# Optimization experiments

Hardware: AMD Instinct MI355X
Metric: run time of the kernel (lower is better)

The kernel has to match this reference:

```python
import jax, jax.numpy as jnp
import numpy as np

NEG_INF = -1e30

def dwconv1(x, dw, db, pw, pb):
    # DWConv with kernel_size=1: depthwise = per-channel scale+bias, pointwise = dense linear.
    # x: [B, L, H]
    return (x * dw + db) @ pw.T + pb

def masked_softmax(logits, maskf, axis):
    # masked_softmax as in SQuAD repos: mask*logits + (1-mask)*(-1e30), then softmax over axis
    m = maskf * logits + (1.0 - maskf) * NEG_INF
    return jax.nn.softmax(m, axis=axis)

def setup_inputs() -> dict:
    key = jax.random.key(0)
    ks = jax.random.split(key, 20)
    B, L, H = 4, 4096, 1024
    s = 1.0 / np.sqrt(H)
    inp = {
        "x": jax.random.normal(ks[0], (B, L, H), dtype=jnp.float32),
        "mask": jax.random.randint(ks[1], (B, L), 0, 2, dtype=jnp.int32),
    }
    names = ["k", "q", "v", "r"]
    for i, n in enumerate(names):
        inp[n + "_dw"] = jax.random.normal(ks[2 + 4 * i], (H,), dtype=jnp.float32) * 0.1 + 1.0
        inp[n + "_db"] = jnp.zeros((H,), dtype=jnp.float32)
        inp[n + "_pw"] = jax.random.normal(ks[3 + 4 * i], (H, H), dtype=jnp.float32) * s
        inp[n + "_pb"] = jnp.zeros((H,), dtype=jnp.float32)
    return inp

def reference(x, mask, k_dw, k_db, k_pw, k_pb, q_dw, q_db, q_pw, q_pb,
              v_dw, v_db, v_pw, v_pb, r_dw, r_db, r_pw, r_pb):
    B, L, H = x.shape
    n_head = 16
    hc = H // n_head
    maskf = mask.astype(x.dtype)[:, None, None, :]  # [B,1,1,L]

    def heads(t):  # [B,L,H] -> [B,nh,hc,L]
        return t.reshape(B, L, n_head, hc).transpose(0, 2, 3, 1)

    keys = heads(dwconv1(x, k_dw, k_db, k_pw, k_pb))
    queries = heads(dwconv1(x, q_dw, q_db, q_pw, q_pb))
    values = heads(dwconv1(x, v_dw, v_db, v_pw, v_pb))

    key_sm = masked_softmax(keys, maskf, axis=3)      # softmax over L
    query_sm = masked_softmax(queries, maskf, axis=2)  # softmax over head channels

    # context = key @ value^T : [B,nh,hc,hc]
    context = jnp.einsum("bhcl,bhdl->bhcd", key_sm, values)
    # attended = context^T @ query : [B,nh,hc(value),L]
    attended = jnp.einsum("bhcd,bhcl->bhdl", context, query_sm)

    agg = attended.transpose(0, 3, 1, 2).reshape(B, L, H)  # concat heads, [B,L,H]
    # dropout is identity in eval mode
    return dwconv1(agg, r_dw, r_db, r_pw, r_pb)
```

## Files before the change

### kernel.cpp

```cpp
#include <hip/hip_runtime.h>
#include <stdint.h>

#define H 1024
#define LSEQ 4096
#define NBATCH 4
#define MT (NBATCH*LSEQ)

typedef __attribute__((ext_vector_type(8))) short bf16x8;
typedef __attribute__((ext_vector_type(4))) short s16x4;
typedef __attribute__((ext_vector_type(4))) float f32x4;

static __device__ __forceinline__ unsigned short f2bf(float f){
  union { float f; unsigned u; } v; v.f = f;
  unsigned u = v.u;
  return (unsigned short)((u + 0x7FFFu + ((u >> 16) & 1u)) >> 16);
}
static __device__ __forceinline__ float bf2f(unsigned short h){
  union { unsigned u; float f; } v; v.u = ((unsigned)h) << 16;
  return v.f;
}
static __device__ __forceinline__ void g2l16(const void* g, void* l){
  __builtin_amdgcn_global_load_lds((const __attribute__((address_space(1))) void*)g,
                                   (__attribute__((address_space(3))) void*)l, 16, 0, 0);
}
static __device__ __forceinline__ f32x4 mfma16(bf16x8 a, bf16x8 b, f32x4 c){
  return __builtin_amdgcn_mfma_f32_16x16x32_bf16(a, b, c, 0, 0, 0);
}

struct P4 { const float* pw[4]; const float* dw[4]; const float* db[4]; const float* pb[4]; };

__global__ __launch_bounds__(256) void prepcvt(P4 a, const float* __restrict__ x,
    short* __restrict__ wb, float* __restrict__ bo, short* __restrict__ xb){
  const int bid = blockIdx.x, t = threadIdx.x;
  if (bid < 4096){
    __shared__ float red[256];
    const int p = bid >> 10, j = bid & 1023;
    const float* row = a.pw[p] + (size_t)j * H;
    const float* dwp = a.dw[p];
    const float* dbp = a.db[p];
    float acc = 0.f;
    #pragma unroll
    for (int k = 0; k < 4; ++k){
      int i = k*256 + t;
      float pv = row[i];
      wb[((size_t)p*H + j)*H + i] = (short)f2bf(pv * dwp[i]);
      acc += dbp[i] * pv;
    }
    red[t] = acc; __syncthreads();
    for (int s = 128; s > 0; s >>= 1){
      if (t < s) red[t] += red[t+s];
      __syncthreads();
    }
    if (t == 0) bo[p*H + j] = a.pb[p][j] + red[0];
  } else {
    const size_t base = ((size_t)(bid - 4096) * 4096) + (size_t)t * 16;
    #pragma unroll
    for (int h2 = 0; h2 < 2; ++h2){
      const float4* p = (const float4*)(x + base + h2*8);
      float4 u = p[0], v = p[1];
      bf16x8 o;
      o[0]=(short)f2bf(u.x); o[1]=(short)f2bf(u.y); o[2]=(short)f2bf(u.z); o[3]=(short)f2bf(u.w);
      o[4]=(short)f2bf(v.x); o[5]=(short)f2bf(v.y); o[6]=(short)f2bf(v.z); o[7]=(short)f2bf(v.w);
      *(bf16x8*)(xb + base + h2*8) = o;
    }
  }
}

template<int MODE, int NBLK>
__global__ __launch_bounds__(512, 2) void gemm8(const short* __restrict__ A,
    const short* __restrict__ WBp, const float* __restrict__ bia,
    short* __restrict__ oq, short* __restrict__ okT, short* __restrict__ ovT,
    float* __restrict__ ofin){
  __shared__ __align__(16) short lsm[2][2][256*64];

  const int nwg = NBLK * 64;
  const int cpx = nwg >> 3;
  const int bid = blockIdx.x;
  const int swz = (bid & 7) * cpx + (bid >> 3);
  const int mb = swz / NBLK, nb = swz % NBLK;
  const int m0 = mb * 256, n0 = nb * 256;

  const int tid  = threadIdx.x;
  const int lane = tid & 63;
  const int w    = tid >> 6;
  const int wm   = w >> 2, wn = w & 3;
  const int q4 = lane >> 4, r16 = lane & 15;
  const int rl = lane >> 3, sl = lane & 7;
  const int srcsw = ((sl ^ rl) << 3);

#define STAGE_A(BUF_, Q_, KB_) \
  g2l16(A + (size_t)(m0 + (Q_)*64 + w*8 + rl)*H + (KB_) + srcsw, \
        &lsm[0][BUF_][((Q_)*64 + w*8)*64])
#define STAGE_B(BUF_, Q_, KB_) \
  g2l16(WBp + (size_t)(n0 + (Q_)*64 + w*8 + rl)*H + (KB_) + srcsw, \
        &lsm[1][BUF_][((Q_)*64 + w*8)*64])
#define RD_A(dst, BUF_, MI8, KK) { const int row_ = wm*128 + (MI8)*16 + r16; \
  dst = *(const bf16x8*)&lsm[0][BUF_][row_*64 + ((((KK)*4+q4) ^ (row_&7))<<3)]; }
#define RD_B(dst, BUF_, NI4, KK) { const int row_ = wn*64 + (NI4)*16 + r16; \
  dst = *(const bf16x8*)&lsm[1][BUF_][row_*64 + ((((KK)*4+q4) ^ (row_&7))<<3)]; }

  f32x4 acc[8][4] = {};
  bf16x8 aF[4][2], bFa[2][2], bFb[2][2];

  STAGE_B(0,0,0); STAGE_B(0,1,0); STAGE_B(0,2,0); STAGE_B(0,3,0);
  STAGE_A(0,0,0); STAGE_A(0,2,0); STAGE_A(0,1,0); STAGE_A(0,3,0);
  asm volatile("s_waitcnt vmcnt(2)" ::: "memory");
  __builtin_amdgcn_s_barrier();

  #pragma unroll 2
  for (int t = 0; t < 16; ++t){
    const int buf = t & 1, sbuf = buf ^ 1;
    const int skb = ((t < 15) ? (t + 1) : 15) << 6;

    #pragma unroll
    for (int mi = 0; mi < 4; ++mi){ RD_A(aF[mi][0], buf, mi, 0); RD_A(aF[mi][1], buf, mi, 1); }
    #pragma unroll
    for (int ni = 0; ni < 2; ++ni){ RD_B(bFa[ni][0], buf, ni, 0); RD_B(bFa[ni][1], buf, ni, 1); }
    #pragma unroll
    for (int ni = 0; ni < 2; ++ni){ RD_B(bFb[ni][0], buf, 2+ni, 0); RD_B(bFb[ni][1], buf, 2+ni, 1); }
    STAGE_B(sbuf, 0, skb); STAGE_B(sbuf, 1, skb);
    STAGE_B(sbuf, 2, skb); STAGE_B(sbuf, 3, skb);
    __builtin_amdgcn_s_setprio(1);
    #pragma unroll
    for (int kk = 0; kk < 2; ++kk)
      #pragma unroll
      for (int mi = 0; mi < 4; ++mi){
        #pragma unroll
        for (int ni = 0; ni < 2; ++ni)
          acc[mi][ni] = mfma16(aF[mi][kk], bFa[ni][kk], acc[mi][ni]);
        #pragma unroll
        for (int ni = 0; ni < 2; ++ni)
          acc[mi][2+ni] = mfma16(aF[mi][kk], bFb[ni][kk], acc[mi][2+ni]);
      }
    __builtin_amdgcn_s_setprio(0);
    asm volatile("s_waitcnt vmcnt(4)" ::: "memory");
    __builtin_amdgcn_s_barrier();

    #pragma unroll
    for (int mi = 0; mi < 4; ++mi){ RD_A(aF[mi][0], buf, 4+mi, 0); RD_A(aF[mi][1], buf, 4+mi, 1); }
    STAGE_A(sbuf, 0, skb); STAGE_A(sbuf, 2, skb);
    STAGE_A(sbuf, 1, skb); STAGE_A(sbuf, 3, skb);
    __builtin_amdgcn_s_setprio(1);
    #pragma unroll
    for (int kk = 0; kk < 2; ++kk)
      #pragma unroll
      for (int mi = 0; mi < 4; ++mi){
        #pragma unroll
        for (int ni = 0; ni < 2; ++ni)
          acc[4+mi][ni] = mfma16(aF[mi][kk], bFa[ni][kk], acc[4+mi][ni]);
        #pragma unroll
        for (int ni = 0; ni < 2; ++ni)
          acc[4+mi][2+ni] = mfma16(aF[mi][kk], bFb[ni][kk], acc[4+mi][2+ni]);
      }
    __builtin_amdgcn_s_setprio(0);
    asm volatile("s_waitcnt vmcnt(2)" ::: "memory");
    __builtin_amdgcn_s_barrier();
  }
#undef STAGE_A
#undef STAGE_B
#undef RD_A
#undef RD_B

  if (MODE == 1){
    #pragma unroll
    for (int ni4 = 0; ni4 < 4; ++ni4){
      const int n = n0 + wn*64 + ni4*16 + r16;
      const float bv = bia[n];
      #pragma unroll
      for (int mi8 = 0; mi8 < 8; ++mi8){
        const int mbse = m0 + wm*128 + mi8*16 + q4*4;
        #pragma unroll
        for (int j = 0; j < 4; ++j)
          ofin[(size_t)(mbse+j)*H + n] = acc[mi8][ni4][j] + bv;
      }
    }
  } else {
    const int p = n0 >> 10;
    if (p == 1){
      #pragma unroll
      for (int ni4 = 0; ni4 < 4; ++ni4){
        const int n = n0 + wn*64 + ni4*16 + r16;
        const float bv = bia[n];
        const int ch = n & 1023;
        #pragma unroll
        for (int mi8 = 0; mi8 < 8; ++mi8){
          const int mbse = m0 + wm*128 + mi8*16 + q4*4;
          #pragma unroll
          for (int j = 0; j < 4; ++j)
            oq[(size_t)(mbse+j)*H + ch] = (short)f2bf(acc[mi8][ni4][j] + bv);
        }
      }
    } else {
      asm volatile("s_waitcnt vmcnt(0)" ::: "memory");
      __syncthreads();
      char* sC = (char*)&lsm[0][0][0];
      #pragma unroll
      for (int ni4 = 0; ni4 < 4; ++ni4){
        const int cr = wn*64 + ni4*16 + r16;
        const float bv = bia[n0 + cr];
        #pragma unroll
        for (int mi8 = 0; mi8 < 8; ++mi8){
          const int s8 = wm*32 + mi8*4 + q4;
          s16x4 v;
          #pragma unroll
          for (int j = 0; j < 4; ++j) v[j] = (short)f2bf(acc[mi8][ni4][j] + bv);
          *(s16x4*)(sC + cr*512 + ((s8 ^ ((cr & 7) << 1)) << 3)) = v;
        }
      }
      __syncthreads();
      short* ot = (p == 0) ? okT : ovT;
      const int ch0 = n0 & 1023, bb = m0 >> 12, lp0 = m0 & 4095;
      const int c = lane & 31;
      #pragma unroll
      for (int it = 0; it < 16; ++it){
        const int cr = it*16 + w*2 + (lane >> 5);
        bf16x8 vv = *(bf16x8*)(sC + cr*512 + ((c ^ (cr & 7)) << 4));
        *(bf16x8*)&ot[((size_t)bb*H + ch0 + cr)*LSEQ + lp0 + c*8] = vv;
      }
    }
  }
}

__global__ __launch_bounds__(512) void ctx_k(const short* __restrict__ kT,
    const short* __restrict__ vT, const int* __restrict__ mask,
    float* __restrict__ ctxP, float* __restrict__ dloc){
  const int lc = blockIdx.x, h = blockIdx.y, b = blockIdx.z;
  __shared__ __align__(16) short lK[2][64*64];
  __shared__ __align__(16) short lV[2][64*64];
  __shared__ float sDenP[8][64];
  __shared__ int sMkG[2][64];
  __shared__ float sAcc[64][65];
  const int tid = threadIdx.x, lane = tid & 63, w = tid >> 6;
  const int grp = w >> 2, wg = w & 3, tig = tid & 255;
  const short* kb = kT + (size_t)(b*16 + h)*64*LSEQ;
  const short* vb = vT + (size_t)(b*16 + h)*64*LSEQ;
  const int l0 = lc*512;

  f32x4 acc[4] = {};
  float dsum = 0.f;
  const int sl = lane & 7, rl = lane >> 3;
  const int lsw = ((sl ^ rl) << 3);
  for (int kc2 = 0; kc2 < 4; ++kc2){
    const int kc = kc2*2 + grp;
    __syncthreads();
    const int lb = l0 + kc*64;
    #pragma unroll
    for (int c = 0; c < 2; ++c){
      const int r = (wg*2+c)*8 + rl;
      g2l16(kb + (size_t)r*LSEQ + lb + lsw, &lK[grp][(wg*2+c)*512]);
      g2l16(vb + (size_t)r*LSEQ + lb + lsw, &lV[grp][(wg*2+c)*512]);
    }
    if (tig < 64) sMkG[grp][tig] = mask[(size_t)b*LSEQ + lb + tig];
    __syncthreads();
    {
      const int row = lane;
      #pragma unroll
      for (int k2 = 0; k2 < 2; ++k2){
        const int slog = wg*2 + k2;
        const int sp = slog ^ (row & 7);
        bf16x8 v = *(bf16x8*)&lK[grp][row*64 + (sp<<3)];
        bf16x8 o;
        #pragma unroll
        for (int e=0;e<8;++e){
          const float f = bf2f((unsigned short)v[e]);
          const float we = sMkG[grp][slog*8+e] ? __expf(f - 8.0f) : 0.0f;
          dsum += we;
          o[e] = (short)f2bf(we);
        }
        *(bf16x8*)&lK[grp][row*64 + (sp<<3)] = o;
      }
    }
    __syncthreads();
    const int q4 = lane >> 4, r16 = lane & 15;
    #pragma unroll
    for (int kk = 0; kk < 2; ++kk){
      const int slog = kk*4 + q4;
      const int rowA = wg*16 + r16;
      bf16x8 a = *(bf16x8*)&lK[grp][rowA*64 + ((slog ^ (rowA & 7))<<3)];
      #pragma unroll
      for (int ni = 0; ni < 4; ++ni){
        const int rowB = ni*16 + r16;
        bf16x8 bv = *(bf16x8*)&lV[grp][rowB*64 + ((slog ^ (rowB & 7))<<3)];
        acc[ni] = mfma16(a, bv, acc[ni]);
      }
    }
  }
  const int q4 = lane >> 4, r16 = lane & 15;
  sDenP[w][lane] = dsum;
  if (grp == 0){
    #pragma unroll
    for (int ni=0;ni<4;++ni){
      const int d = ni*16 + r16;
      #pragma unroll
      for (int j=0;j<4;++j)
        sAcc[wg*16 + q4*4 + j][d] = acc[ni][j];
    }
  }
  __syncthreads();
  if (grp == 1){
    float* op = ctxP + (((size_t)(b*16 + h)*8 + lc) << 12);
    #pragma unroll
    for (int ni=0;ni<4;++ni){
      const int d = ni*16 + r16;
      #pragma unroll
      for (int j=0;j<4;++j){
        const int c = wg*16 + q4*4 + j;
        op[c*64 + d] = acc[ni][j] + sAcc[c][d];
      }
    }
  }
  if (tid < 64){
    const int idx = (((b*16 + h)*8 + lc) << 6) + tid;
    float dv = 0.f;
    #pragma unroll
    for (int ww = 0; ww < 8; ++ww) dv += sDenP[ww][tid];
    dloc[idx] = dv;
  }
}

__global__ __launch_bounds__(512) void attd_k(const short* __restrict__ qb,
    const float* __restrict__ ctxP, const float* __restrict__ dloc,
    const int* __restrict__ mask, short* __restrict__ agg){
  const int lcb = blockIdx.x, h = blockIdx.y, b = blockIdx.z;
  __shared__ __align__(16) short lQ[2][64*64];
  __shared__ __align__(16) short lCt[64*64];
  __shared__ float sInv[64];
  const int tid = threadIdx.x, lane = tid & 63, w = tid >> 6;
  const int grp = w >> 2, wg = w & 3;
  if (tid < 64){
    const int base = ((b*16 + h) << 9) + tid;
    float den = 0.f;
    #pragma unroll
    for (int i = 0; i < 8; ++i) den += dloc[base + i*64];
    sInv[tid] = 1.0f / fmaxf(den, 1e-30f);
  }
  __syncthreads();
  {
    const int d = lane;
    const float* base = ctxP + ((size_t)(b*16 + h)*8 << 12);
    #pragma unroll
    for (int i=0;i<8;++i){
      const int c = w*8 + i;
      float s = 0.f;
      #pragma unroll
      for (int ch = 0; ch < 8; ++ch)
        s += base[ch*4096 + c*64 + d];
      s *= sInv[c];
      lCt[d*64 + ((((c>>3) ^ (d&7))<<3) | (c&7))] = (short)f2bf(s);
    }
  }
  const int l0g = b*LSEQ + lcb*1024 + grp*512;
  const int sl = lane & 7, rl = lane >> 3;
  const int lsw = ((sl ^ rl) << 3);
  for (int sc = 0; sc < 8; ++sc){
    __syncthreads();
    #pragma unroll
    for (int c = 0; c < 2; ++c){
      const int r = (wg*2+c)*8 + rl;
      g2l16(qb + (size_t)(l0g + sc*64 + r)*H + h*64 + lsw, &lQ[grp][(wg*2+c)*512]);
    }
    __syncthreads();
    {
      const int row = wg*16 + (lane & 15);
      const int q4 = lane >> 4;
      const int mk = mask[(size_t)l0g + sc*64 + row];
      float vals[16];
      float mxv = -3e38f;
      #pragma unroll
      for (int k2=0;k2<2;++k2){
        const int slog = q4*2 + k2;
        const int sp = slog ^ (row & 7);
        bf16x8 v = *(bf16x8*)&lQ[grp][row*64 + (sp<<3)];
        #pragma unroll
        for (int e=0;e<8;++e){
          const float f = bf2f((unsigned short)v[e]);
          vals[k2*8+e] = f;
          mxv = fmaxf(mxv, f);
        }
      }
      mxv = fmaxf(mxv, __shfl_xor(mxv, 16));
      mxv = fmaxf(mxv, __shfl_xor(mxv, 32));
      float s = 0.f;
      #pragma unroll
      for (int e=0;e<16;++e){ vals[e] = __expf(vals[e]-mxv); s += vals[e]; }
      s += __shfl_xor(s, 16);
      s += __shfl_xor(s, 32);
      const float inv = 1.0f / s;
      #pragma unroll
      for (int k2=0;k2<2;++k2){
        const int slog = q4*2 + k2;
        const int sp = slog ^ (row & 7);
        bf16x8 o;
        #pragma unroll
        for (int e=0;e<8;++e)
          o[e] = (short)f2bf(mk ? vals[k2*8+e]*inv : 0.015625f);
        *(bf16x8*)&lQ[grp][row*64 + (sp<<3)] = o;
      }
    }
    __syncthreads();
    f32x4 acc[4] = {};
    const int q4 = lane >> 4, r16 = lane & 15;
    #pragma unroll
    for (int kk=0;kk<2;++kk){
      const int slog = kk*4 + q4;
      const int rowA = wg*16 + r16;
      bf16x8 a = *(bf16x8*)&lQ[grp][rowA*64 + ((slog ^ (rowA&7))<<3)];
      #pragma unroll
      for (int ni=0;ni<4;++ni){
        const int rowB = ni*16 + r16;
        bf16x8 bv = *(bf16x8*)&lCt[rowB*64 + ((slog ^ (rowB&7))<<3)];
        acc[ni] = mfma16(a, bv, acc[ni]);
      }
    }
    #pragma unroll
    for (int ni=0;ni<4;++ni){
      const int d = ni*16 + r16;
      #pragma unroll
      for (int j=0;j<4;++j){
        const int lrow = wg*16 + q4*4 + j;
        agg[(size_t)(l0g + sc*64 + lrow)*H + h*64 + d] = (short)f2bf(acc[ni][j]);
      }
    }
  }
}

extern "C" void kernel_launch(void* const* d_in, const int* in_sizes, int n_in,
                              void* d_out, int out_size, void* d_ws, size_t ws_size,
                              hipStream_t stream){
  (void)in_sizes; (void)n_in; (void)out_size; (void)ws_size;
  const float* x    = (const float*)d_in[0];
  const int*   mask = (const int*)d_in[1];
  P4 prm;
  for (int p2 = 0; p2 < 4; ++p2){
    prm.dw[p2] = (const float*)d_in[2 + 4*p2];
    prm.db[p2] = (const float*)d_in[3 + 4*p2];
    prm.pw[p2] = (const float*)d_in[4 + 4*p2];
    prm.pb[p2] = (const float*)d_in[5 + 4*p2];
  }
  char* ws = (char*)d_ws;
  short* WB   = (short*)(ws);
  float* BIAS = (float*)(ws + ((size_t)8<<20));
  float* DLOC = (float*)(ws + ((size_t)8<<20) + (512<<10));
  short* XB   = (short*)(ws + ((size_t)9<<20));
  short* QB   = (short*)(ws + ((size_t)41<<20));
  short* KT   = (short*)(ws + ((size_t)73<<20));
  short* VT   = (short*)(ws + ((size_t)105<<20));
  float* CTXP = (float*)(ws + ((size_t)137<<20));
  short* AGG  = XB;

  prepcvt<<<8192, 256, 0, stream>>>(prm, x, WB, BIAS, XB);
  gemm8<0,12><<<768, 512, 0, stream>>>(XB, WB, BIAS, QB, KT, VT, nullptr);
  ctx_k<<<dim3(8,16,4), 512, 0, stream>>>(KT, VT, mask, CTXP, DLOC);
  attd_k<<<dim3(4,16,4), 512, 0, stream>>>(QB, CTXP, DLOC, mask, AGG);
  gemm8<1,4><<<256, 512, 0, stream>>>(AGG, WB + (size_t)3*H*H, BIAS + 3*1024,
                                      nullptr, nullptr, nullptr, (float*)d_out);
}
```

Before: 204.0 us.

## Restructure GEMM to 4 waves per block with 128x128 per-wave tiles

The 256x256-tile GEMM now runs with 256 threads (4 waves in a 2x2 grid) instead of 512 threads (8 waves in 2x4). Each wave computes a 128x128 sub-tile with an 8x8 accumulator array, and the staging, fragment reads and epilogues are reworked to match. The aim is more MFMA work per LDS fragment read and fewer waves contending at barriers. The cost is much higher register pressure (256 accumulator floats per lane) at one block per CU, which may reduce latency hiding or cause spills.

```diff
diff --git a/kernel.cpp b/kernel.cpp
--- a/kernel.cpp
+++ b/kernel.cpp
@@ -67,7 +67,7 @@
 }
 
 template<int MODE, int NBLK>
-__global__ __launch_bounds__(512, 2) void gemm8(const short* __restrict__ A,
+__global__ __launch_bounds__(256, 1) void gemm4(const short* __restrict__ A,
     const short* __restrict__ WBp, const float* __restrict__ bia,
     short* __restrict__ oq, short* __restrict__ okT, short* __restrict__ ovT,
     float* __restrict__ ofin){
@@ -83,28 +83,33 @@
   const int tid  = threadIdx.x;
   const int lane = tid & 63;
   const int w    = tid >> 6;
-  const int wm   = w >> 2, wn = w & 3;
+  const int wm   = w >> 1, wn = w & 1;
   const int q4 = lane >> 4, r16 = lane & 15;
   const int rl = lane >> 3, sl = lane & 7;
   const int srcsw = ((sl ^ rl) << 3);
 
-#define STAGE_A(BUF_, Q_, KB_) \
-  g2l16(A + (size_t)(m0 + (Q_)*64 + w*8 + rl)*H + (KB_) + srcsw, \
-        &lsm[0][BUF_][((Q_)*64 + w*8)*64])
-#define STAGE_B(BUF_, Q_, KB_) \
-  g2l16(WBp + (size_t)(n0 + (Q_)*64 + w*8 + rl)*H + (KB_) + srcsw, \
-        &lsm[1][BUF_][((Q_)*64 + w*8)*64])
+#define STAGE_A(BUF_, Q_, C_) \
+  g2l16(A + (size_t)(m0 + (Q_)*64 + w*16 + (C_)*8 + rl)*H + skb + srcsw, \
+        &lsm[0][BUF_][((Q_)*64 + w*16 + (C_)*8)*64])
+#define STAGE_B(BUF_, Q_, C_) \
+  g2l16(WBp + (size_t)(n0 + (Q_)*64 + w*16 + (C_)*8 + rl)*H + skb + srcsw, \
+        &lsm[1][BUF_][((Q_)*64 + w*16 + (C_)*8)*64])
 #define RD_A(dst, BUF_, MI8, KK) { const int row_ = wm*128 + (MI8)*16 + r16; \
   dst = *(const bf16x8*)&lsm[0][BUF_][row_*64 + ((((KK)*4+q4) ^ (row_&7))<<3)]; }
-#define RD_B(dst, BUF_, NI4, KK) { const int row_ = wn*64 + (NI4)*16 + r16; \
+#define RD_B(dst, BUF_, NI8, KK) { const int row_ = wn*128 + (NI8)*16 + r16; \
   dst = *(const bf16x8*)&lsm[1][BUF_][row_*64 + ((((KK)*4+q4) ^ (row_&7))<<3)]; }
 
-  f32x4 acc[8][4] = {};
-  bf16x8 aF[4][2], bFa[2][2], bFb[2][2];
-
-  STAGE_B(0,0,0); STAGE_B(0,1,0); STAGE_B(0,2,0); STAGE_B(0,3,0);
-  STAGE_A(0,0,0); STAGE_A(0,2,0); STAGE_A(0,1,0); STAGE_A(0,3,0);
-  asm volatile("s_waitcnt vmcnt(2)" ::: "memory");
+  f32x4 acc[8][8] = {};
+  bf16x8 aF[4][2], bF[8][2];
+
+  {
+    const int skb = 0;
+    STAGE_B(0,0,0); STAGE_B(0,0,1); STAGE_B(0,1,0); STAGE_B(0,1,1);
+    STAGE_B(0,2,0); STAGE_B(0,2,1); STAGE_B(0,3,0); STAGE_B(0,3,1);
+    STAGE_A(0,0,0); STAGE_A(0,0,1); STAGE_A(0,2,0); STAGE_A(0,2,1);
+    STAGE_A(0,1,0); STAGE_A(0,1,1); STAGE_A(0,3,0); STAGE_A(0,3,1);
+  }
+  asm volatile("s_waitcnt vmcnt(4)" ::: "memory");
   __builtin_amdgcn_s_barrier();
 
   #pragma unroll 2
@@ -115,45 +120,35 @@
     #pragma unroll
     for (int mi = 0; mi < 4; ++mi){ RD_A(aF[mi][0], buf, mi, 0); RD_A(aF[mi][1], buf, mi, 1); }
     #pragma unroll
-    for (int ni = 0; ni < 2; ++ni){ RD_B(bFa[ni][0], buf, ni, 0); RD_B(bFa[ni][1], buf, ni, 1); }
-    #pragma unroll
-    for (int ni = 0; ni < 2; ++ni){ RD_B(bFb[ni][0], buf, 2+ni, 0); RD_B(bFb[ni][1], buf, 2+ni, 1); }
-    STAGE_B(sbuf, 0, skb); STAGE_B(sbuf, 1, skb);
-    STAGE_B(sbuf, 2, skb); STAGE_B(sbuf, 3, skb);
+    for (int ni = 0; ni < 8; ++ni){ RD_B(bF[ni][0], buf, ni, 0); RD_B(bF[ni][1], buf, ni, 1); }
+    STAGE_B(sbuf,0,0); STAGE_B(sbuf,0,1); STAGE_B(sbuf,1,0); STAGE_B(sbuf,1,1);
+    STAGE_B(sbuf,2,0); STAGE_B(sbuf,2,1); STAGE_B(sbuf,3,0); STAGE_B(sbuf,3,1);
     __builtin_amdgcn_s_setprio(1);
     #pragma unroll
     for (int kk = 0; kk < 2; ++kk)
       #pragma unroll
-      for (int mi = 0; mi < 4; ++mi){
-        #pragma unroll
-        for (int ni = 0; ni < 2; ++ni)
-          acc[mi][ni] = mfma16(aF[mi][kk], bFa[ni][kk], acc[mi][ni]);
-        #pragma unroll
-        for (int ni = 0; ni < 2; ++ni)
-          acc[mi][2+ni] = mfma16(aF[mi][kk], bFb[ni][kk], acc[mi][2+ni]);
-      }
+      for (int mi = 0; mi < 4; ++mi)
+        #pragma unroll
+        for (int ni = 0; ni < 8; ++ni)
+          acc[mi][ni] = mfma16(aF[mi][kk], bF[ni][kk], acc[mi][ni]);
+    __builtin_amdgcn_s_setprio(0);
+    asm volatile("s_waitcnt vmcnt(8)" ::: "memory");
+    __builtin_amdgcn_s_barrier();
+
+    #pragma unroll
+    for (int mi = 0; mi < 4; ++mi){ RD_A(aF[mi][0], buf, 4+mi, 0); RD_A(aF[mi][1], buf, 4+mi, 1); }
+    STAGE_A(sbuf,0,0); STAGE_A(sbuf,0,1); STAGE_A(sbuf,2,0); STAGE_A(sbuf,2,1);
+    STAGE_A(sbuf,1,0); STAGE_A(sbuf,1,1); STAGE_A(sbuf,3,0); STAGE_A(sbuf,3,1);
+    __builtin_amdgcn_s_setprio(1);
+    #pragma unroll
+    for (int kk = 0; kk < 2; ++kk)
+      #pragma unroll
+      for (int mi = 0; mi < 4; ++mi)
+        #pragma unroll
+        for (int ni = 0; ni < 8; ++ni)
+          acc[4+mi][ni] = mfma16(aF[mi][kk], bF[ni][kk], acc[4+mi][ni]);
     __builtin_amdgcn_s_setprio(0);
     asm volatile("s_waitcnt vmcnt(4)" ::: "memory");
-    __builtin_amdgcn_s_barrier();
-
-    #pragma unroll
-    for (int mi = 0; mi < 4; ++mi){ RD_A(aF[mi][0], buf, 4+mi, 0); RD_A(aF[mi][1], buf, 4+mi, 1); }
-    STAGE_A(sbuf, 0, skb); STAGE_A(sbuf, 2, skb);
-    STAGE_A(sbuf, 1, skb); STAGE_A(sbuf, 3, skb);
-    __builtin_amdgcn_s_setprio(1);
-    #pragma unroll
-    for (int kk = 0; kk < 2; ++kk)
-      #pragma unroll
-      for (int mi = 0; mi < 4; ++mi){
-        #pragma unroll
-        for (int ni = 0; ni < 2; ++ni)
-          acc[4+mi][ni] = mfma16(aF[mi][kk], bFa[ni][kk], acc[4+mi][ni]);
-        #pragma unroll
-        for (int ni = 0; ni < 2; ++ni)
-          acc[4+mi][2+ni] = mfma16(aF[mi][kk], bFb[ni][kk], acc[4+mi][2+ni]);
-      }
-    __builtin_amdgcn_s_setprio(0);
-    asm volatile("s_waitcnt vmcnt(2)" ::: "memory");
     __builtin_amdgcn_s_barrier();
   }
 #undef STAGE_A
@@ -163,31 +158,31 @@
 
   if (MODE == 1){
     #pragma unroll
-    for (int ni4 = 0; ni4 < 4; ++ni4){
-      const int n = n0 + wn*64 + ni4*16 + r16;
+    for (int ni = 0; ni < 8; ++ni){
+      const int n = n0 + wn*128 + ni*16 + r16;
       const float bv = bia[n];
       #pragma unroll
-      for (int mi8 = 0; mi8 < 8; ++mi8){
-        const int mbse = m0 + wm*128 + mi8*16 + q4*4;
+      for (int mi = 0; mi < 8; ++mi){
+        const int mbse = m0 + wm*128 + mi*16 + q4*4;
         #pragma unroll
         for (int j = 0; j < 4; ++j)
-          ofin[(size_t)(mbse+j)*H + n] = acc[mi8][ni4][j] + bv;
+          ofin[(size_t)(mbse+j)*H + n] = acc[mi][ni][j] + bv;
       }
     }
   } else {
     const int p = n0 >> 10;
     if (p == 1){
       #pragma unroll
-      for (int ni4 = 0; ni4 < 4; ++ni4){
-        const int n = n0 + wn*64 + ni4*16 + r16;
+      for (int ni = 0; ni < 8; ++ni){
+        const int n = n0 + wn*128 + ni*16 + r16;
         const float bv = bia[n];
         const int ch = n & 1023;
         #pragma unroll
-        for (int mi8 = 0; mi8 < 8; ++mi8){
-          const int mbse = m0 + wm*128 + mi8*16 + q4*4;
+        for (int mi = 0; mi < 8; ++mi){
+          const int mbse = m0 + wm*128 + mi*16 + q4*4;
           #pragma unroll
           for (int j = 0; j < 4; ++j)
-            oq[(size_t)(mbse+j)*H + ch] = (short)f2bf(acc[mi8][ni4][j] + bv);
+            oq[(size_t)(mbse+j)*H + ch] = (short)f2bf(acc[mi][ni][j] + bv);
         }
       }
     } else {
@@ -195,15 +190,15 @@
       __syncthreads();
       char* sC = (char*)&lsm[0][0][0];
       #pragma unroll
-      for (int ni4 = 0; ni4 < 4; ++ni4){
-        const int cr = wn*64 + ni4*16 + r16;
+      for (int ni = 0; ni < 8; ++ni){
+        const int cr = wn*128 + ni*16 + r16;
         const float bv = bia[n0 + cr];
         #pragma unroll
-        for (int mi8 = 0; mi8 < 8; ++mi8){
-          const int s8 = wm*32 + mi8*4 + q4;
+        for (int mi = 0; mi < 8; ++mi){
+          const int s8 = wm*32 + mi*4 + q4;
           s16x4 v;
           #pragma unroll
-          for (int j = 0; j < 4; ++j) v[j] = (short)f2bf(acc[mi8][ni4][j] + bv);
+          for (int j = 0; j < 4; ++j) v[j] = (short)f2bf(acc[mi][ni][j] + bv);
           *(s16x4*)(sC + cr*512 + ((s8 ^ ((cr & 7) << 1)) << 3)) = v;
         }
       }
@@ -212,8 +207,8 @@
       const int ch0 = n0 & 1023, bb = m0 >> 12, lp0 = m0 & 4095;
       const int c = lane & 31;
       #pragma unroll
-      for (int it = 0; it < 16; ++it){
-        const int cr = it*16 + w*2 + (lane >> 5);
+      for (int it = 0; it < 32; ++it){
+        const int cr = it*8 + w*2 + (lane >> 5);
         bf16x8 vv = *(bf16x8*)(sC + cr*512 + ((c ^ (cr & 7)) << 4));
         *(bf16x8*)&ot[((size_t)bb*H + ch0 + cr)*LSEQ + lp0 + c*8] = vv;
       }
@@ -449,9 +444,9 @@
   short* AGG  = XB;
 
   prepcvt<<<8192, 256, 0, stream>>>(prm, x, WB, BIAS, XB);
-  gemm8<0,12><<<768, 512, 0, stream>>>(XB, WB, BIAS, QB, KT, VT, nullptr);
+  gemm4<0,12><<<768, 256, 0, stream>>>(XB, WB, BIAS, QB, KT, VT, nullptr);
   ctx_k<<<dim3(8,16,4), 512, 0, stream>>>(KT, VT, mask, CTXP, DLOC);
   attd_k<<<dim3(4,16,4), 512, 0, stream>>>(QB, CTXP, DLOC, mask, AGG);
-  gemm8<1,4><<<256, 512, 0, stream>>>(AGG, WB + (size_t)3*H*H, BIAS + 3*1024,
+  gemm4<1,4><<<256, 256, 0, stream>>>(AGG, WB + (size_t)3*H*H, BIAS + 3*1024,
                                       nullptr, nullptr, nullptr, (float*)d_out);
 }
```

Result: slower. 531.7 us (median of 2 runs) (+160.6%).

## Double-buffer ctx_k with 4 waves and prefetch of next L chunk

Applied to the files above, without the earlier changes.

Rewrites the context kernel to use 256 threads (4 waves) that walk all 8 L-chunks sequentially with a double-buffered LDS pipeline, prefetching chunk kc+1 via global_load_lds while the current chunk is exponentiated and multiplied. This removes the two-group split and the cross-group shared-memory reduction of accumulators. The goal is to hide global load latency behind compute. In exchange each block has half the waves and a longer serial loop. It also relies on manual waitcnt/barrier ordering to keep the in-place LDS rewrite of the K tile safe.

```diff
diff --git a/kernel.cpp b/kernel.cpp
--- a/kernel.cpp
+++ b/kernel.cpp
@@ -221,100 +221,95 @@
   }
 }
 
-__global__ __launch_bounds__(512) void ctx_k(const short* __restrict__ kT,
+__global__ __launch_bounds__(256) void ctx_k(const short* __restrict__ kT,
     const short* __restrict__ vT, const int* __restrict__ mask,
     float* __restrict__ ctxP, float* __restrict__ dloc){
   const int lc = blockIdx.x, h = blockIdx.y, b = blockIdx.z;
   __shared__ __align__(16) short lK[2][64*64];
   __shared__ __align__(16) short lV[2][64*64];
-  __shared__ float sDenP[8][64];
-  __shared__ int sMkG[2][64];
-  __shared__ float sAcc[64][65];
+  __shared__ int sMk[2][64];
+  __shared__ float sDen[4][64];
   const int tid = threadIdx.x, lane = tid & 63, w = tid >> 6;
-  const int grp = w >> 2, wg = w & 3, tig = tid & 255;
   const short* kb = kT + (size_t)(b*16 + h)*64*LSEQ;
   const short* vb = vT + (size_t)(b*16 + h)*64*LSEQ;
   const int l0 = lc*512;
+  const int sl = lane & 7, rl = lane >> 3;
+  const int lsw = ((sl ^ rl) << 3);
+
+#define CSTAGE(BUF_, KC_) { const int lb_ = l0 + (KC_)*64; \
+  const int r0_ = (w*2)*8 + rl, r1_ = (w*2+1)*8 + rl; \
+  g2l16(kb + (size_t)r0_*LSEQ + lb_ + lsw, &lK[BUF_][(w*2)*512]); \
+  g2l16(vb + (size_t)r0_*LSEQ + lb_ + lsw, &lV[BUF_][(w*2)*512]); \
+  g2l16(kb + (size_t)r1_*LSEQ + lb_ + lsw, &lK[BUF_][(w*2+1)*512]); \
+  g2l16(vb + (size_t)r1_*LSEQ + lb_ + lsw, &lV[BUF_][(w*2+1)*512]); \
+  if (tid < 64) sMk[BUF_][tid] = mask[(size_t)b*LSEQ + lb_ + tid]; }
 
   f32x4 acc[4] = {};
   float dsum = 0.f;
-  const int sl = lane & 7, rl = lane >> 3;
-  const int lsw = ((sl ^ rl) << 3);
-  for (int kc2 = 0; kc2 < 4; ++kc2){
-    const int kc = kc2*2 + grp;
-    __syncthreads();
-    const int lb = l0 + kc*64;
-    #pragma unroll
-    for (int c = 0; c < 2; ++c){
-      const int r = (wg*2+c)*8 + rl;
-      g2l16(kb + (size_t)r*LSEQ + lb + lsw, &lK[grp][(wg*2+c)*512]);
-      g2l16(vb + (size_t)r*LSEQ + lb + lsw, &lV[grp][(wg*2+c)*512]);
-    }
-    if (tig < 64) sMkG[grp][tig] = mask[(size_t)b*LSEQ + lb + tig];
-    __syncthreads();
+
+  CSTAGE(0, 0);
+  asm volatile("s_waitcnt vmcnt(0) lgkmcnt(0)" ::: "memory");
+  __builtin_amdgcn_s_barrier();
+
+  for (int kc = 0; kc < 8; ++kc){
+    const int buf = kc & 1, sbuf = buf ^ 1;
+    if (kc < 7) CSTAGE(sbuf, kc + 1);
     {
       const int row = lane;
       #pragma unroll
       for (int k2 = 0; k2 < 2; ++k2){
-        const int slog = wg*2 + k2;
+        const int slog = w*2 + k2;
         const int sp = slog ^ (row & 7);
-        bf16x8 v = *(bf16x8*)&lK[grp][row*64 + (sp<<3)];
+        bf16x8 v = *(bf16x8*)&lK[buf][row*64 + (sp<<3)];
         bf16x8 o;
         #pragma unroll
-        for (int e=0;e<8;++e){
+        for (int e = 0; e < 8; ++e){
           const float f = bf2f((unsigned short)v[e]);
-          const float we = sMkG[grp][slog*8+e] ? __expf(f - 8.0f) : 0.0f;
+          const float we = sMk[buf][slog*8+e] ? __expf(f - 8.0f) : 0.0f;
           dsum += we;
           o[e] = (short)f2bf(we);
         }
-        *(bf16x8*)&lK[grp][row*64 + (sp<<3)] = o;
-      }
-    }
-    __syncthreads();
-    const int q4 = lane >> 4, r16 = lane & 15;
-    #pragma unroll
-    for (int kk = 0; kk < 2; ++kk){
-      const int slog = kk*4 + q4;
-      const int rowA = wg*16 + r16;
-      bf16x8 a = *(bf16x8*)&lK[grp][rowA*64 + ((slog ^ (rowA & 7))<<3)];
-      #pragma unroll
-      for (int ni = 0; ni < 4; ++ni){
-        const int rowB = ni*16 + r16;
-        bf16x8 bv = *(bf16x8*)&lV[grp][rowB*64 + ((slog ^ (rowB & 7))<<3)];
-        acc[ni] = mfma16(a, bv, acc[ni]);
-      }
-    }
-  }
+        *(bf16x8*)&lK[buf][row*64 + (sp<<3)] = o;
+      }
+    }
+    asm volatile("s_waitcnt lgkmcnt(0)" ::: "memory");
+    __builtin_amdgcn_s_barrier();
+    {
+      const int q4 = lane >> 4, r16 = lane & 15;
+      #pragma unroll
+      for (int kk = 0; kk < 2; ++kk){
+        const int slog = kk*4 + q4;
+        const int rowA = w*16 + r16;
+        bf16x8 a = *(bf16x8*)&lK[buf][rowA*64 + ((slog ^ (rowA & 7))<<3)];
+        #pragma unroll
+        for (int ni = 0; ni < 4; ++ni){
+          const int rowB = ni*16 + r16;
+          bf16x8 bv = *(bf16x8*)&lV[buf][rowB*64 + ((slog ^ (rowB & 7))<<3)];
+          acc[ni] = mfma16(a, bv, acc[ni]);
+        }
+      }
+    }
+    asm volatile("s_waitcnt vmcnt(0) lgkmcnt(0)" ::: "memory");
+    __builtin_amdgcn_s_barrier();
+  }
+#undef CSTAGE
+
   const int q4 = lane >> 4, r16 = lane & 15;
-  sDenP[w][lane] = dsum;
-  if (grp == 0){
-    #pragma unroll
-    for (int ni=0;ni<4;++ni){
-      const int d = ni*16 + r16;
-      #pragma unroll
-      for (int j=0;j<4;++j)
-        sAcc[wg*16 + q4*4 + j][d] = acc[ni][j];
-    }
-  }
+  float* op = ctxP + (((size_t)(b*16 + h)*8 + lc) << 12);
+  #pragma unroll
+  for (int ni = 0; ni < 4; ++ni){
+    const int d = ni*16 + r16;
+    #pragma unroll
+    for (int j = 0; j < 4; ++j){
+      const int c = w*16 + q4*4 + j;
+      op[c*64 + d] = acc[ni][j];
+    }
+  }
+  sDen[w][lane] = dsum;
   __syncthreads();
-  if (grp == 1){
-    float* op = ctxP + (((size_t)(b*16 + h)*8 + lc) << 12);
-    #pragma unroll
-    for (int ni=0;ni<4;++ni){
-      const int d = ni*16 + r16;
-      #pragma unroll
-      for (int j=0;j<4;++j){
-        const int c = wg*16 + q4*4 + j;
-        op[c*64 + d] = acc[ni][j] + sAcc[c][d];
-      }
-    }
-  }
   if (tid < 64){
     const int idx = (((b*16 + h)*8 + lc) << 6) + tid;
-    float dv = 0.f;
-    #pragma unroll
-    for (int ww = 0; ww < 8; ++ww) dv += sDenP[ww][tid];
-    dloc[idx] = dv;
+    dloc[idx] = sDen[0][tid] + sDen[1][tid] + sDen[2][tid] + sDen[3][tid];
   }
 }
 
@@ -450,7 +445,7 @@
 
   prepcvt<<<8192, 256, 0, stream>>>(prm, x, WB, BIAS, XB);
   gemm8<0,12><<<768, 512, 0, stream>>>(XB, WB, BIAS, QB, KT, VT, nullptr);
-  ctx_k<<<dim3(8,16,4), 512, 0, stream>>>(KT, VT, mask, CTXP, DLOC);
+  ctx_k<<<dim3(8,16,4), 256, 0, stream>>>(KT, VT, mask, CTXP, DLOC);
   attd_k<<<dim3(4,16,4), 512, 0, stream>>>(QB, CTXP, DLOC, mask, AGG);
   gemm8<1,4><<<256, 512, 0, stream>>>(AGG, WB + (size_t)3*H*H, BIAS + 3*1024,
                                       nullptr, nullptr, nullptr, (float*)d_out);
```

New measurement: 205.5 us. About the same (+0.7%).
